# Kernel optimization log

Measured on AMD Instinct MI355X. Metric: run time of the kernel, lower is better.

Reference implementation:

```python
import jax, jax.numpy as jnp
import numpy as np

N_SAMPLES, N_TIME, N_FEAT = 64, 4, 64
N_ENTITIES = 10000
D = N_TIME * N_FEAT  # 256
K = 10


def setup_inputs() -> dict:
    key = jax.random.key(0)
    k1, k2 = jax.random.split(key)
    query = jax.random.uniform(k1, (N_SAMPLES, N_TIME, N_FEAT), dtype=jnp.float32)
    # module state: self.enity_info, flattened view must be [n_entities, D]
    enity_info = jax.random.uniform(k2, (N_ENTITIES, D), dtype=jnp.float32)
    return {"query": query, "enity_info": enity_info, "k": K}


def reference(query, enity_info, k):
    n_samples = query.shape[0]
    q = query.reshape(n_samples, -1)                 # [n, d]
    e = enity_info.reshape(enity_info.shape[0], -1)  # [m, d]
    # pairwise Jaccard: sum(min) / sum(max) over feature dim
    inter = jnp.sum(jnp.minimum(q[:, None, :], e[None, :, :]), axis=2)  # [n, m]
    union = jnp.sum(jnp.maximum(q[:, None, :], e[None, :, :]), axis=2)  # [n, m]
    jaccard = inter / union                                             # [n, m]
    # torch.topk largest=True, sorted=True -> lax.top_k (descending)
    _, top_idx = jax.lax.top_k(jaccard, k)
    # torch.topk largest=False, sorted=True -> ascending smallest: top_k of negated
    _, bot_idx = jax.lax.top_k(-jaccard, k)
    return top_idx, bot_idx
```

## Files before the change

### kernel.cpp

```cpp
#include <hip/hip_runtime.h>
#include <math.h>
#include <limits.h>

#define NQ     64
#define NE     10000
#define K      10
#define NSTRIP 250
#define EPB    40
#define TPB    1024
#define EPP    5
#define SLOT   11
#define SCALE  8388608.0f

__device__ __forceinline__ bool better_top(double v, int i, double v2, int i2) {
    return (v > v2) || (v == v2 && i < i2);
}
__device__ __forceinline__ bool better_bot(double v, int i, double v2, int i2) {
    return (v < v2) || (v == v2 && i < i2);
}

template <bool TOP>
__device__ __forceinline__ void merge_slots16(double* Mv, unsigned short* Mi, int A, int B) {
    double ov[K]; unsigned short oi[K];
    int a = 0, b = 0;
#pragma unroll
    for (int o = 0; o < K; ++o) {
        double va = Mv[A * SLOT + a]; int ia = Mi[A * SLOT + a];
        double vb = Mv[B * SLOT + b]; int ib = Mi[B * SLOT + b];
        bool pick = TOP ? better_top(va, ia, vb, ib) : better_bot(va, ia, vb, ib);
        ov[o] = pick ? va : vb;
        oi[o] = (unsigned short)(pick ? ia : ib);
        if (pick) ++a; else ++b;
    }
#pragma unroll
    for (int o = 0; o < K; ++o) { Mv[A * SLOT + o] = ov[o]; Mi[A * SLOT + o] = oi[o]; }
}

#define CSWAP(CMP, v, ii, A, B)                                            \
    {                                                                      \
        bool c_ = CMP(v[B], ii[B], v[A], ii[A]);                           \
        double tv_ = c_ ? v[B] : v[A]; double uv_ = c_ ? v[A] : v[B];      \
        int    ti_ = c_ ? ii[B] : ii[A]; int ui_ = c_ ? ii[A] : ii[B];     \
        v[A] = tv_; v[B] = uv_; ii[A] = ti_; ii[B] = ui_;                  \
    }
#define SORT5(CMP, v, ii)            \
    CSWAP(CMP, v, ii, 0, 1) CSWAP(CMP, v, ii, 3, 4) CSWAP(CMP, v, ii, 2, 4) \
    CSWAP(CMP, v, ii, 2, 3) CSWAP(CMP, v, ii, 0, 3) CSWAP(CMP, v, ii, 0, 2) \
    CSWAP(CMP, v, ii, 1, 4) CSWAP(CMP, v, ii, 1, 3) CSWAP(CMP, v, ii, 1, 2)

__global__ __launch_bounds__(256) void ent_sums(const float* __restrict__ E,
                                                unsigned* __restrict__ Se) {
    const int w = threadIdx.x >> 6, l = threadIdx.x & 63;
    const int j = blockIdx.x * 4 + w;
    float4 v = reinterpret_cast<const float4*>(E)[(size_t)j * 64 + l];
    unsigned s = (unsigned)(v.x * SCALE) + (unsigned)(v.y * SCALE)
               + (unsigned)(v.z * SCALE) + (unsigned)(v.w * SCALE);
#pragma unroll
    for (int m = 1; m < 64; m <<= 1) s += (unsigned)__shfl_xor((int)s, m, 64);
    if (l == 0) Se[j] = s;
}

__global__ __launch_bounds__(TPB, 4) void jac_part(
        const float* __restrict__ Q, const float* __restrict__ E,
        const unsigned* __restrict__ Se,
        double* __restrict__ pvT, double* __restrict__ pvB,
        int* __restrict__ piT, int* __restrict__ piB) {
    __shared__ uint4 QT[2][2048];
    __shared__ uint4 EB[16][EPP][65];

    const int t    = threadIdx.x;
    const int l    = t & 63;
    const int w    = t >> 6;
    const int q    = l >> 1;
    const int sub  = l & 1;
    const int half = w & 1;
    const int p    = w >> 1;
    const int strip = blockIdx.x;
    const int q64  = half * 32 + q;

    unsigned* SqP = (unsigned*)&EB[0][0][0];
    {
        const int sq = t >> 4, c = t & 15;
        unsigned acc = 0;
#pragma unroll
        for (int r = 0; r < 4; ++r) {
            const int gg = c + 16 * r;
            float4 v = reinterpret_cast<const float4*>(Q)[sq * 64 + gg];
            uint4 u;
            u.x = (unsigned)(v.x * SCALE); u.y = (unsigned)(v.y * SCALE);
            u.z = (unsigned)(v.z * SCALE); u.w = (unsigned)(v.w * SCALE);
            QT[sq >> 5][(gg & 31) * 64 + 2 * (sq & 31) + (gg >> 5)] = u;
            acc += u.x + u.y + u.z + u.w;
        }
        SqP[t] = acc;
    }
    __syncthreads();
    unsigned Sq = 0;
#pragma unroll
    for (int pp = 0; pp < 16; ++pp) Sq += SqP[q64 * 16 + ((pp + q64) & 15)];
    __syncthreads();

    const uint4* QTt = &QT[half][0];
    const int jb = strip * EPB;
    const float4* E4 = (const float4*)E;

#pragma unroll
    for (int s = 0; s < EPP; ++s) {
        float4 er = E4[(size_t)(jb + p + 8 * s) * 64 + l];
        uint4 eu;
        eu.x = (unsigned)(er.x * SCALE); eu.y = (unsigned)(er.y * SCALE);
        eu.z = (unsigned)(er.z * SCALE); eu.w = (unsigned)(er.w * SCALE);
        EB[w][s][l + (l >> 5)] = eu;
    }
    unsigned se[EPP];
#pragma unroll
    for (int s = 0; s < EPP; ++s) se[s] = Se[jb + p + 8 * s];

    const uint4* ebr = &EB[w][0][sub * 33];
    unsigned a0[EPP], a1[EPP];
#pragma unroll
    for (int s = 0; s < EPP; ++s) { a0[s] = 0; a1[s] = 0; }

#pragma unroll 4
    for (int g = 0; g < 32; ++g) {
        uint4 qv = QTt[g * 64 + l];
#pragma unroll
        for (int s = 0; s < EPP; ++s) {
            uint4 ev = ebr[s * 65 + g];
            a0[s] += min(qv.x, ev.x) + min(qv.y, ev.y);
            a1[s] += min(qv.z, ev.z) + min(qv.w, ev.w);
        }
    }

    unsigned recI[EPP], recU[EPP];
#pragma unroll
    for (int s = 0; s < EPP; ++s) {
        unsigned ih = a0[s] + a1[s];
        unsigned inter = ih + (unsigned)__shfl_xor((int)ih, 1, 64);
        recI[s] = inter;
        recU[s] = Sq + se[s] - inter;
    }

    double jv[EPP]; int ji[EPP];
#pragma unroll
    for (int s = 0; s < EPP; ++s) {
        jv[s] = (double)recI[s] / (double)recU[s];
        ji[s] = jb + p + 8 * s;
    }
    double av[EPP]; int ai[EPP]; double bv[EPP]; int bi[EPP];
#pragma unroll
    for (int s = 0; s < EPP; ++s) { av[s] = jv[s]; ai[s] = ji[s]; bv[s] = jv[s]; bi[s] = ji[s]; }
    SORT5(better_top, av, ai)
    SORT5(better_bot, bv, bi)

    __syncthreads();
    double*         Mv = ((double*)&QT[0][0]) + half * (256 * SLOT);
    unsigned short* Mi = ((unsigned short*)&EB[0][0][0]) + half * (256 * SLOT);
    const int slot = p * 32 + q;

    if (sub == 0) {
#pragma unroll
        for (int o = 0; o < EPP; ++o) { Mv[slot * SLOT + o] = av[o]; Mi[slot * SLOT + o] = (unsigned short)ai[o]; }
#pragma unroll
        for (int o = EPP; o < K; ++o) { Mv[slot * SLOT + o] = -INFINITY; Mi[slot * SLOT + o] = 0xFFFFu; }
    }
    __syncthreads();
    for (int s = 4; s >= 1; s >>= 1) {
        if (sub == 0 && p < s) merge_slots16<true>(Mv, Mi, p * 32 + q, (p + s) * 32 + q);
        __syncthreads();
    }
    if (sub == 0 && p == 0) {
        const size_t off = ((size_t)q64 * NSTRIP + strip) * K;
#pragma unroll
        for (int o = 0; o < K; ++o) { pvT[off + o] = Mv[q * SLOT + o]; piT[off + o] = (int)Mi[q * SLOT + o]; }
    }
    __syncthreads();

    if (sub == 0) {
#pragma unroll
        for (int o = 0; o < EPP; ++o) { Mv[slot * SLOT + o] = bv[o]; Mi[slot * SLOT + o] = (unsigned short)bi[o]; }
#pragma unroll
        for (int o = EPP; o < K; ++o) { Mv[slot * SLOT + o] = INFINITY; Mi[slot * SLOT + o] = 0xFFFFu; }
    }
    __syncthreads();
    for (int s = 4; s >= 1; s >>= 1) {
        if (sub == 0 && p < s) merge_slots16<false>(Mv, Mi, p * 32 + q, (p + s) * 32 + q);
        __syncthreads();
    }
    if (sub == 0 && p == 0) {
        const size_t off = ((size_t)q64 * NSTRIP + strip) * K;
#pragma unroll
        for (int o = 0; o < K; ++o) { pvB[off + o] = Mv[q * SLOT + o]; piB[off + o] = (int)Mi[q * SLOT + o]; }
    }
}

__global__ __launch_bounds__(256) void final_extract(
        const double* __restrict__ pvT, const double* __restrict__ pvB,
        const int* __restrict__ piT, const int* __restrict__ piB,
        int* __restrict__ out) {
    __shared__ double Lv[NSTRIP * K];
    __shared__ int    Li[NSTRIP * K];
    __shared__ double Wv[4];
    __shared__ int    Wi[4], Wo[4];
    __shared__ int    res[K];

    const int b   = blockIdx.x;
    const int q   = b >> 1;
    const bool top = (b & 1) == 0;
    const int t   = threadIdx.x;
    const int l   = t & 63;
    const int w   = t >> 6;

    const double* V = (top ? pvT : pvB) + (size_t)q * NSTRIP * K;
    const int*    I = (top ? piT : piB) + (size_t)q * NSTRIP * K;

    for (int i = t; i < NSTRIP * K; i += 256) {
        double v = V[i];
        Lv[i] = top ? v : -v;
        Li[i] = I[i];
    }
    __syncthreads();

    int h = 0;
    double hv = (t < NSTRIP) ? Lv[t * K] : -INFINITY;
    int    hi = (t < NSTRIP) ? Li[t * K] : INT_MAX;

    for (int r = 0; r < K; ++r) {
        double v = hv; int idx = hi; int own = t;
#pragma unroll
        for (int m = 1; m < 64; m <<= 1) {
            double ov = __shfl_xor(v, m, 64);
            int    oi = __shfl_xor(idx, m, 64);
            int    oo = __shfl_xor(own, m, 64);
            if (better_top(ov, oi, v, idx)) { v = ov; idx = oi; own = oo; }
        }
        if (l == 0) { Wv[w] = v; Wi[w] = idx; Wo[w] = own; }
        __syncthreads();
        double gv = Wv[0]; int gi = Wi[0], go = Wo[0];
#pragma unroll
        for (int ww = 1; ww < 4; ++ww)
            if (better_top(Wv[ww], Wi[ww], gv, gi)) { gv = Wv[ww]; gi = Wi[ww]; go = Wo[ww]; }
        if (t == go) {
            ++h;
            bool ok = h < K;
            hv = ok ? Lv[t * K + h] : -INFINITY;
            hi = ok ? Li[t * K + h] : INT_MAX;
        }
        if (t == 0) res[r] = gi;
        __syncthreads();
    }

    if (t < K) out[(top ? 0 : NQ * K) + q * K + t] = res[t];
}

extern "C" void kernel_launch(void* const* d_in, const int* in_sizes, int n_in,
                              void* d_out, int out_size, void* d_ws, size_t ws_size,
                              hipStream_t stream) {
    const float* Q = (const float*)d_in[0];
    const float* E = (const float*)d_in[1];
    int* out = (int*)d_out;

    char* ws = (char*)d_ws;
    unsigned* Se  = (unsigned*)(ws);
    double*   pvT = (double*)(ws + 40960);
    double*   pvB = (double*)(ws + 1320960);
    int*      piT = (int*)   (ws + 2600960);
    int*      piB = (int*)   (ws + 3240960);

    hipLaunchKernelGGL(ent_sums, dim3(NE / 4), dim3(256), 0, stream, E, Se);
    hipLaunchKernelGGL(jac_part, dim3(NSTRIP), dim3(TPB), 0, stream,
                       Q, E, Se, pvT, pvB, piT, piB);
    hipLaunchKernelGGL(final_extract, dim3(NQ * 2), dim3(256), 0, stream,
                       pvT, pvB, piT, piB, out);
}
```

Before: 47.50 us.

## Split query halves across blocks and merge top and bottom lists concurrently

The Jaccard partial kernel now launches two 512-thread blocks per entity strip, one per half of the queries, where before a single 1024-thread block covered both halves. The bottom-k list is stored negated, so both lists use one comparator, and the two lanes of each pair merge the top and bottom lists in parallel in separate shared buffers. This halves the serial merge phases and the barriers between them, and spreads the work over more blocks. In exchange, every entity strip is loaded from global memory and converted twice, and occupancy is now bounded per 512-thread block.

Result: faster. 45.16 us (-4.9%).

```diff
diff --git a/kernel.cpp b/kernel.cpp
--- a/kernel.cpp
+++ b/kernel.cpp
@@ -7,7 +7,7 @@
 #define K      10
 #define NSTRIP 250
 #define EPB    40
-#define TPB    1024
+#define TPB    512
 #define EPP    5
 #define SLOT   11
 #define SCALE  8388608.0f
@@ -15,11 +15,7 @@
 __device__ __forceinline__ bool better_top(double v, int i, double v2, int i2) {
     return (v > v2) || (v == v2 && i < i2);
 }
-__device__ __forceinline__ bool better_bot(double v, int i, double v2, int i2) {
-    return (v < v2) || (v == v2 && i < i2);
-}
-
-template <bool TOP>
+
 __device__ __forceinline__ void merge_slots16(double* Mv, unsigned short* Mi, int A, int B) {
     double ov[K]; unsigned short oi[K];
     int a = 0, b = 0;
@@ -27,7 +23,7 @@
     for (int o = 0; o < K; ++o) {
         double va = Mv[A * SLOT + a]; int ia = Mi[A * SLOT + a];
         double vb = Mv[B * SLOT + b]; int ib = Mi[B * SLOT + b];
-        bool pick = TOP ? better_top(va, ia, vb, ib) : better_bot(va, ia, vb, ib);
+        bool pick = better_top(va, ia, vb, ib);
         ov[o] = pick ? va : vb;
         oi[o] = (unsigned short)(pick ? ia : ib);
         if (pick) ++a; else ++b;
@@ -36,17 +32,18 @@
     for (int o = 0; o < K; ++o) { Mv[A * SLOT + o] = ov[o]; Mi[A * SLOT + o] = oi[o]; }
 }
 
-#define CSWAP(CMP, v, ii, A, B)                                            \
+
+#define CSWAP(v, ii, A, B)                                                 \
     {                                                                      \
-        bool c_ = CMP(v[B], ii[B], v[A], ii[A]);                           \
+        bool c_ = better_top(v[B], ii[B], v[A], ii[A]);                    \
         double tv_ = c_ ? v[B] : v[A]; double uv_ = c_ ? v[A] : v[B];      \
         int    ti_ = c_ ? ii[B] : ii[A]; int ui_ = c_ ? ii[A] : ii[B];     \
         v[A] = tv_; v[B] = uv_; ii[A] = ti_; ii[B] = ui_;                  \
     }
-#define SORT5(CMP, v, ii)            \
-    CSWAP(CMP, v, ii, 0, 1) CSWAP(CMP, v, ii, 3, 4) CSWAP(CMP, v, ii, 2, 4) \
-    CSWAP(CMP, v, ii, 2, 3) CSWAP(CMP, v, ii, 0, 3) CSWAP(CMP, v, ii, 0, 2) \
-    CSWAP(CMP, v, ii, 1, 4) CSWAP(CMP, v, ii, 1, 3) CSWAP(CMP, v, ii, 1, 2)
+#define SORT5(v, ii)            \
+    CSWAP(v, ii, 0, 1) CSWAP(v, ii, 3, 4) CSWAP(v, ii, 2, 4) \
+    CSWAP(v, ii, 2, 3) CSWAP(v, ii, 0, 3) CSWAP(v, ii, 0, 2) \
+    CSWAP(v, ii, 1, 4) CSWAP(v, ii, 1, 3) CSWAP(v, ii, 1, 2)
 
 __global__ __launch_bounds__(256) void ent_sums(const float* __restrict__ E,
                                                 unsigned* __restrict__ Se) {
@@ -60,23 +57,22 @@
     if (l == 0) Se[j] = s;
 }
 
-__global__ __launch_bounds__(TPB, 4) void jac_part(
+__global__ __launch_bounds__(TPB, 2) void jac_part(
         const float* __restrict__ Q, const float* __restrict__ E,
         const unsigned* __restrict__ Se,
         double* __restrict__ pvT, double* __restrict__ pvB,
         int* __restrict__ piT, int* __restrict__ piB) {
-    __shared__ uint4 QT[2][2048];
-    __shared__ uint4 EB[16][EPP][65];
+    __shared__ uint4 QT[2048];
+    __shared__ uint4 EB[8][EPP][65];
 
     const int t    = threadIdx.x;
     const int l    = t & 63;
     const int w    = t >> 6;
     const int q    = l >> 1;
     const int sub  = l & 1;
-    const int half = w & 1;
-    const int p    = w >> 1;
-    const int strip = blockIdx.x;
-    const int q64  = half * 32 + q;
+    const int strip = blockIdx.x >> 1;
+    const int qbase = (blockIdx.x & 1) * 32;
+    const int q64  = qbase + q;
 
     unsigned* SqP = (unsigned*)&EB[0][0][0];
     {
@@ -85,11 +81,11 @@
 #pragma unroll
         for (int r = 0; r < 4; ++r) {
             const int gg = c + 16 * r;
-            float4 v = reinterpret_cast<const float4*>(Q)[sq * 64 + gg];
+            float4 v = reinterpret_cast<const float4*>(Q)[(qbase + sq) * 64 + gg];
             uint4 u;
             u.x = (unsigned)(v.x * SCALE); u.y = (unsigned)(v.y * SCALE);
             u.z = (unsigned)(v.z * SCALE); u.w = (unsigned)(v.w * SCALE);
-            QT[sq >> 5][(gg & 31) * 64 + 2 * (sq & 31) + (gg >> 5)] = u;
+            QT[(gg & 31) * 64 + 2 * sq + (gg >> 5)] = u;
             acc += u.x + u.y + u.z + u.w;
         }
         SqP[t] = acc;
@@ -97,16 +93,15 @@
     __syncthreads();
     unsigned Sq = 0;
 #pragma unroll
-    for (int pp = 0; pp < 16; ++pp) Sq += SqP[q64 * 16 + ((pp + q64) & 15)];
-    __syncthreads();
-
-    const uint4* QTt = &QT[half][0];
+    for (int pp = 0; pp < 16; ++pp) Sq += SqP[q * 16 + ((pp + q) & 15)];
+    __syncthreads();
+
     const int jb = strip * EPB;
     const float4* E4 = (const float4*)E;
 
 #pragma unroll
     for (int s = 0; s < EPP; ++s) {
-        float4 er = E4[(size_t)(jb + p + 8 * s) * 64 + l];
+        float4 er = E4[(size_t)(jb + w + 8 * s) * 64 + l];
         uint4 eu;
         eu.x = (unsigned)(er.x * SCALE); eu.y = (unsigned)(er.y * SCALE);
         eu.z = (unsigned)(er.z * SCALE); eu.w = (unsigned)(er.w * SCALE);
@@ -114,7 +109,7 @@
     }
     unsigned se[EPP];
 #pragma unroll
-    for (int s = 0; s < EPP; ++s) se[s] = Se[jb + p + 8 * s];
+    for (int s = 0; s < EPP; ++s) se[s] = Se[jb + w + 8 * s];
 
     const uint4* ebr = &EB[w][0][sub * 33];
     unsigned a0[EPP], a1[EPP];
@@ -123,7 +118,7 @@
 
 #pragma unroll 4
     for (int g = 0; g < 32; ++g) {
-        uint4 qv = QTt[g * 64 + l];
+        uint4 qv = QT[g * 64 + l];
 #pragma unroll
         for (int s = 0; s < EPP; ++s) {
             uint4 ev = ebr[s * 65 + g];
@@ -132,65 +127,47 @@
         }
     }
 
-    unsigned recI[EPP], recU[EPP];
+    double av[EPP]; int ai[EPP]; double bv[EPP]; int bi[EPP];
 #pragma unroll
     for (int s = 0; s < EPP; ++s) {
         unsigned ih = a0[s] + a1[s];
         unsigned inter = ih + (unsigned)__shfl_xor((int)ih, 1, 64);
-        recI[s] = inter;
-        recU[s] = Sq + se[s] - inter;
-    }
-
-    double jv[EPP]; int ji[EPP];
-#pragma unroll
-    for (int s = 0; s < EPP; ++s) {
-        jv[s] = (double)recI[s] / (double)recU[s];
-        ji[s] = jb + p + 8 * s;
-    }
-    double av[EPP]; int ai[EPP]; double bv[EPP]; int bi[EPP];
-#pragma unroll
-    for (int s = 0; s < EPP; ++s) { av[s] = jv[s]; ai[s] = ji[s]; bv[s] = jv[s]; bi[s] = ji[s]; }
-    SORT5(better_top, av, ai)
-    SORT5(better_bot, bv, bi)
-
-    __syncthreads();
-    double*         Mv = ((double*)&QT[0][0]) + half * (256 * SLOT);
-    unsigned short* Mi = ((unsigned short*)&EB[0][0][0]) + half * (256 * SLOT);
-    const int slot = p * 32 + q;
-
-    if (sub == 0) {
-#pragma unroll
-        for (int o = 0; o < EPP; ++o) { Mv[slot * SLOT + o] = av[o]; Mi[slot * SLOT + o] = (unsigned short)ai[o]; }
-#pragma unroll
-        for (int o = EPP; o < K; ++o) { Mv[slot * SLOT + o] = -INFINITY; Mi[slot * SLOT + o] = 0xFFFFu; }
-    }
-    __syncthreads();
+        unsigned uni   = Sq + se[s] - inter;
+        double jac = (double)inter / (double)uni;
+        av[s] = jac;  ai[s] = jb + w + 8 * s;
+        bv[s] = -jac; bi[s] = ai[s];
+    }
+    SORT5(av, ai)
+    SORT5(bv, bi)
+
+    __syncthreads();
+    double*         MvA = (double*)&QT[0];
+    unsigned short* MiA = (unsigned short*)((char*)&QT[0] + 22528);
+    double*         MvB = (double*)&EB[0][0][0];
+    unsigned short* MiB = (unsigned short*)((char*)&EB[0][0][0] + 22528);
+    double*         Mv  = sub ? MvB : MvA;
+    unsigned short* Mi  = sub ? MiB : MiA;
+    const int slot = w * 32 + q;
+
+#pragma unroll
+    for (int o = 0; o < EPP; ++o) {
+        Mv[slot * SLOT + o] = sub ? bv[o] : av[o];
+        Mi[slot * SLOT + o] = (unsigned short)(sub ? bi[o] : ai[o]);
+    }
+#pragma unroll
+    for (int o = EPP; o < K; ++o) { Mv[slot * SLOT + o] = -INFINITY; Mi[slot * SLOT + o] = 0xFFFFu; }
+    __syncthreads();
+
     for (int s = 4; s >= 1; s >>= 1) {
-        if (sub == 0 && p < s) merge_slots16<true>(Mv, Mi, p * 32 + q, (p + s) * 32 + q);
-        __syncthreads();
-    }
-    if (sub == 0 && p == 0) {
+        if (w < s) merge_slots16(Mv, Mi, w * 32 + q, (w + s) * 32 + q);
+        if (s > 1) __syncthreads();
+    }
+    if (w == 0) {
         const size_t off = ((size_t)q64 * NSTRIP + strip) * K;
-#pragma unroll
-        for (int o = 0; o < K; ++o) { pvT[off + o] = Mv[q * SLOT + o]; piT[off + o] = (int)Mi[q * SLOT + o]; }
-    }
-    __syncthreads();
-
-    if (sub == 0) {
-#pragma unroll
-        for (int o = 0; o < EPP; ++o) { Mv[slot * SLOT + o] = bv[o]; Mi[slot * SLOT + o] = (unsigned short)bi[o]; }
-#pragma unroll
-        for (int o = EPP; o < K; ++o) { Mv[slot * SLOT + o] = INFINITY; Mi[slot * SLOT + o] = 0xFFFFu; }
-    }
-    __syncthreads();
-    for (int s = 4; s >= 1; s >>= 1) {
-        if (sub == 0 && p < s) merge_slots16<false>(Mv, Mi, p * 32 + q, (p + s) * 32 + q);
-        __syncthreads();
-    }
-    if (sub == 0 && p == 0) {
-        const size_t off = ((size_t)q64 * NSTRIP + strip) * K;
-#pragma unroll
-        for (int o = 0; o < K; ++o) { pvB[off + o] = Mv[q * SLOT + o]; piB[off + o] = (int)Mi[q * SLOT + o]; }
+        double* pv = sub ? pvB : pvT;
+        int*    pi = sub ? piB : piT;
+#pragma unroll
+        for (int o = 0; o < K; ++o) { pv[off + o] = Mv[q * SLOT + o]; pi[off + o] = (int)Mi[q * SLOT + o]; }
     }
 }
 
@@ -215,8 +192,7 @@
     const int*    I = (top ? piT : piB) + (size_t)q * NSTRIP * K;
 
     for (int i = t; i < NSTRIP * K; i += 256) {
-        double v = V[i];
-        Lv[i] = top ? v : -v;
+        Lv[i] = V[i];
         Li[i] = I[i];
     }
     __syncthreads();
@@ -268,7 +244,7 @@
     int*      piB = (int*)   (ws + 3240960);
 
     hipLaunchKernelGGL(ent_sums, dim3(NE / 4), dim3(256), 0, stream, E, Se);
-    hipLaunchKernelGGL(jac_part, dim3(NSTRIP), dim3(TPB), 0, stream,
+    hipLaunchKernelGGL(jac_part, dim3(NSTRIP * 2), dim3(TPB), 0, stream,
                        Q, E, Se, pvT, pvB, piT, piB);
     hipLaunchKernelGGL(final_extract, dim3(NQ * 2), dim3(256), 0, stream,
                        pvT, pvB, piT, piB, out);
```
